# Kernel optimization log

Measured on AMD Instinct MI355X. Metric: run time of the kernel, lower is better.

The kernel has to match this reference:

```python
import jax, jax.numpy as jnp
import numpy as np

NH = 32      # num_attention_heads
HD = 128     # head dim (kv_channels)
NG = 2       # multi_query_group_num
LAYER_NUMBER = 1


def apply_rotary_pos_emb(x, rope_cache):
    # x: [b, np, sq, hn]; rope_cache: [1, sq_max, rot/2, 2]
    b, nh, sq, hn = x.shape
    rot_dim = rope_cache.shape[-2] * 2
    xr, x_pass = x[..., :rot_dim], x[..., rot_dim:]
    xs = xr.reshape(b, nh, sq, rot_dim // 2, 2)
    c = rope_cache[:, :sq].reshape(-1, 1, sq, rot_dim // 2, 2)
    out = jnp.stack(
        [xs[..., 0] * c[..., 0] - xs[..., 1] * c[..., 1],
         xs[..., 1] * c[..., 0] + xs[..., 0] * c[..., 1]], axis=-1)
    out = out.reshape(b, nh, sq, rot_dim)
    return jnp.concatenate([out, x_pass], axis=-1)


def setup_inputs() -> dict:
    key = jax.random.key(0)
    ks = jax.random.split(key, 5)
    b, sq, h = 2, 2048, 4096
    qkv_out = NH * HD + 2 * NG * HD  # 4608
    return {
        "hidden_states": jax.random.normal(ks[0], (b, sq, h), jnp.float32),
        "rope_cache": jax.random.normal(ks[1], (1, sq, HD // 4, 2), jnp.float32),
        "W_qkv": jax.random.normal(ks[2], (h, qkv_out), jnp.float32) * 0.02,
        "b_qkv": jax.random.normal(ks[3], (qkv_out,), jnp.float32) * 0.02,
        "W_dense": jax.random.normal(ks[4], (NH * HD, h), jnp.float32) * 0.02,
    }


def reference(hidden_states, rope_cache, W_qkv, b_qkv, W_dense):
    b, sq, h = hidden_states.shape
    mixed = hidden_states @ W_qkv + b_qkv  # [b, sq, nh*hd + 2*ng*hd]
    q_sz = NH * HD
    kv_sz = NG * HD
    q = mixed[..., :q_sz].reshape(b, sq, NH, HD).transpose(0, 2, 1, 3)          # [b,nh,sq,hd]
    k = mixed[..., q_sz:q_sz + kv_sz].reshape(b, sq, NG, HD).transpose(0, 2, 1, 3)  # [b,ng,sq,hd]
    v = mixed[..., q_sz + kv_sz:].reshape(b, sq, NG, HD).transpose(0, 2, 1, 3)      # [b,ng,sq,hd]

    q = apply_rotary_pos_emb(q, rope_cache)
    k = apply_rotary_pos_emb(k, rope_cache)

    # expand KV groups to full heads (multi-query attention)
    rep = NH // NG
    k = jnp.broadcast_to(k[:, :, None], (b, NG, rep, sq, HD)).reshape(b, NH, sq, HD)
    v = jnp.broadcast_to(v[:, :, None], (b, NG, rep, sq, HD)).reshape(b, NH, sq, HD)

    # CoreAttention (eager path, fp32 softmax, causal)
    coeff = float(max(1, LAYER_NUMBER))  # apply_query_key_layer_scaling
    norm_factor = np.sqrt(HD) * coeff
    scores = jnp.einsum("bhqd,bhkd->bhqk", q, k) / norm_factor
    scores = scores.astype(jnp.float32) * coeff
    causal = jnp.tril(jnp.ones((sq, sq), dtype=bool))
    scores = jnp.where(causal[None, None], scores, -jnp.inf)
    probs = jax.nn.softmax(scores, axis=-1).astype(v.dtype)
    context = jnp.einsum("bhqk,bhkd->bhqd", probs, v)   # [b,nh,sq,hd]
    context = context.transpose(0, 2, 1, 3).reshape(b, sq, NH * HD)
    return context @ W_dense
```

## Files before the change

kernel.cpp:

```cpp
#include <hip/hip_runtime.h>
#include <hip/hip_bf16.h>
#include <stdint.h>

#define B_    2
#define SQ    2048
#define H_    4096
#define NHEAD 32
#define HDIM  128
#define NGRP  2
#define QKVN  4608
#define SCALE 0.08838834764831845f
#define QSCALE (0.08838834764831845f * 1.4426950408889634f)

typedef __attribute__((ext_vector_type(8))) short bf16x8;
typedef __attribute__((ext_vector_type(4))) short bf16x4;
typedef __attribute__((ext_vector_type(4))) float f32x4;

__device__ __forceinline__ float b2f(short s) {
  union { float f; unsigned u; } x; x.u = ((unsigned)(unsigned short)s) << 16; return x.f;
}
__device__ __forceinline__ short f2b(float f) {
  union { float f; unsigned u; } x; x.f = f;
  unsigned r = x.u + 0x7fffu + ((x.u >> 16) & 1u);
  return (short)(r >> 16);
}
__device__ __forceinline__ void gll16(const void* g, void* l) {
  __builtin_amdgcn_global_load_lds(
      (const __attribute__((address_space(1))) unsigned int*)g,
      (__attribute__((address_space(3))) unsigned int*)l, 16, 0, 0);
}

__global__ void conv_f32_bf16(const float* __restrict__ x, short* __restrict__ y, int n) {
  int i = (blockIdx.x * blockDim.x + threadIdx.x) * 4;
  if (i >= n) return;
  float4 v = *(const float4*)(x + i);
  union { short s[4]; uint2 u; } o;
  o.s[0] = f2b(v.x); o.s[1] = f2b(v.y); o.s[2] = f2b(v.z); o.s[3] = f2b(v.w);
  *(uint2*)(y + i) = o.u;
}

__global__ void transpose_f32_bf16(const float* __restrict__ W, short* __restrict__ Wt,
                                   int R, int C) {
  __shared__ float tile[32][33];
  int c0 = blockIdx.x * 32, r0 = blockIdx.y * 32;
  int tx = threadIdx.x, ty = threadIdx.y;
  #pragma unroll
  for (int i = 0; i < 32; i += 8)
    tile[ty + i][tx] = W[(size_t)(r0 + ty + i) * C + c0 + tx];
  __syncthreads();
  #pragma unroll
  for (int i = 0; i < 32; i += 8)
    Wt[(size_t)(c0 + ty + i) * R + r0 + tx] = f2b(tile[tx][ty + i]);
}

template<bool BIAS, bool OUTF32>
__global__ __launch_bounds__(256, 2) void gemm_bf16(
    const short* __restrict__ A, const short* __restrict__ Bt,
    const float* __restrict__ bias, short* __restrict__ outb,
    float* __restrict__ outf, int M, int N, int K)
{
  __shared__ short smA[128 * 64];
  __shared__ short smB[128 * 64];
  const int t = threadIdx.x;
  const int l = t & 63;
  const int w = t >> 6;
  const int wr = w >> 1, wc = w & 1;
  const int m0 = blockIdx.y * 128, n0 = blockIdx.x * 128;

  const f32x4 z = {0.f, 0.f, 0.f, 0.f};
  f32x4 acc[4][4];
  #pragma unroll
  for (int m = 0; m < 4; ++m)
    #pragma unroll
    for (int n = 0; n < 4; ++n) acc[m][n] = z;

  for (int k0 = 0; k0 < K; k0 += 64) {
    __syncthreads();
    #pragma unroll
    for (int i = 0; i < 4; ++i) {
      int c = t + i * 256;
      int row = c >> 3, slot = c & 7;
      int ss = slot ^ (row & 7);
      gll16(A  + (size_t)(m0 + row) * K + k0 + ss * 8,
            (char*)smA + (i * 256 + w * 64) * 16);
      gll16(Bt + (size_t)(n0 + row) * K + k0 + ss * 8,
            (char*)smB + (i * 256 + w * 64) * 16);
    }
    __syncthreads();
    #pragma unroll
    for (int kk = 0; kk < 2; ++kk) {
      bf16x8 a[4], b[4];
      #pragma unroll
      for (int m = 0; m < 4; ++m) {
        int row = wr * 64 + m * 16 + (l & 15);
        int off = (kk * 64 + ((l >> 4) << 4)) ^ ((row & 7) << 4);
        a[m] = *(const bf16x8*)((const char*)smA + row * 128 + off);
      }
      #pragma unroll
      for (int n = 0; n < 4; ++n) {
        int row = wc * 64 + n * 16 + (l & 15);
        int off = (kk * 64 + ((l >> 4) << 4)) ^ ((row & 7) << 4);
        b[n] = *(const bf16x8*)((const char*)smB + row * 128 + off);
      }
      #pragma unroll
      for (int m = 0; m < 4; ++m)
        #pragma unroll
        for (int n = 0; n < 4; ++n)
          acc[m][n] = __builtin_amdgcn_mfma_f32_16x16x32_bf16(a[m], b[n], acc[m][n], 0, 0, 0);
    }
  }

  #pragma unroll
  for (int m = 0; m < 4; ++m) {
    int row = m0 + wr * 64 + m * 16 + ((l >> 4) << 2);
    #pragma unroll
    for (int n = 0; n < 4; ++n) {
      int col = n0 + wc * 64 + n * 16 + (l & 15);
      float bv = BIAS ? bias[col] : 0.f;
      #pragma unroll
      for (int j = 0; j < 4; ++j) {
        float vv = acc[m][n][j] + bv;
        if (OUTF32) outf[(size_t)(row + j) * N + col] = vv;
        else        outb[(size_t)(row + j) * N + col] = f2b(vv);
      }
    }
  }
}

__global__ __launch_bounds__(512, 2) void gemm256(
    const short* __restrict__ A, const short* __restrict__ Bt,
    float* __restrict__ outf, int M, int N, int K, int nbx)
{
  __shared__ char sm[131072];
  const int t = threadIdx.x, l = t & 63, w = t >> 6;
  const int lq = l & 15, hi = l >> 4;
  const int wm = w >> 2, wn = w & 3;
  const int nwg = (int)gridDim.x;
  const int oid = (int)blockIdx.x;
  const int swz = (oid & 7) * (nwg >> 3) + (oid >> 3);
  const int by = swz / nbx, bx = swz - by * nbx;
  const int m0 = by * 256, n0 = bx * 256;
  const int nkt = K >> 6;

  auto stage = [&](int tt, int r) {
    int kb = (tt < nkt ? tt : tt - nkt) << 6;
    const short* src = (r < 2) ? Bt + (size_t)(n0 + (r << 7)) * K + kb
                               : A  + (size_t)(m0 + ((r - 2) << 7)) * K + kb;
    char* dst = sm + ((tt & 1) << 16) + (r >= 2 ? 0 : 32768) + ((r & 1) << 14);
    #pragma unroll
    for (int i = 0; i < 2; ++i) {
      int c = (i << 9) + t;
      int row = c >> 3, ss = (c & 7) ^ (row & 7);
      gll16(src + (size_t)row * K + ss * 8, dst + ((i << 9) + (w << 6)) * 16);
    }
  };
  bf16x8 aC[2][2], bC[4][2];
  auto ldA = [&](int b, int q, bf16x8 (&out)[2][2]) {
    #pragma unroll
    for (int fr = 0; fr < 2; ++fr) {
      int ra = wm * 128 + q * 32 + fr * 16 + lq;
      #pragma unroll
      for (int kk = 0; kk < 2; ++kk)
        out[fr][kk] = *(const bf16x8*)(sm + (b << 16) + ra * 128 + (((kk << 2) + hi) ^ (ra & 7)) * 16);
    }
  };
  auto ldB = [&](int b, bf16x8 (&out)[4][2]) {
    #pragma unroll
    for (int fc = 0; fc < 4; ++fc) {
      int rb = wn * 64 + fc * 16 + lq;
      #pragma unroll
      for (int kk = 0; kk < 2; ++kk)
        out[fc][kk] = *(const bf16x8*)(sm + (b << 16) + 32768 + rb * 128 + (((kk << 2) + hi) ^ (rb & 7)) * 16);
    }
  };

  const f32x4 z = {0.f, 0.f, 0.f, 0.f};
  f32x4 acc[8][4];
  #pragma unroll
  for (int i = 0; i < 8; ++i)
    #pragma unroll
    for (int j = 0; j < 4; ++j) acc[i][j] = z;

  stage(0, 0); stage(0, 1); stage(0, 2); stage(0, 3);
  stage(1, 0); stage(1, 1); stage(1, 2);
  asm volatile("s_waitcnt vmcnt(6)" ::: "memory");
  __builtin_amdgcn_s_barrier();
  ldB(0, bC); ldA(0, 0, aC);
  asm volatile("s_waitcnt lgkmcnt(0)" ::: "memory");

#define GPHASE(p, STG_T, STG_R)                                           \
  {                                                                       \
    stage((STG_T), (STG_R));                                              \
    __builtin_amdgcn_sched_barrier(0);                                    \
    __builtin_amdgcn_s_barrier();                                         \
    __builtin_amdgcn_s_setprio(1);                                        \
    _Pragma("unroll")                                                     \
    for (int kk = 0; kk < 2; ++kk)                                        \
      _Pragma("unroll")                                                   \
      for (int fr = 0; fr < 2; ++fr)                                      \
        _Pragma("unroll")                                                 \
        for (int fc = 0; fc < 4; ++fc)                                    \
          acc[(p) * 2 + fr][fc] = __builtin_amdgcn_mfma_f32_16x16x32_bf16(\
              aC[fr][kk], bC[fc][kk], acc[(p) * 2 + fr][fc], 0, 0, 0);    \
    __builtin_amdgcn_s_setprio(0);                                        \
    if ((p) < 3) ldA(bsel, (p) + 1, aC);                                  \
    else { ldA(bsel ^ 1, 0, aC); ldB(bsel ^ 1, bC); }                     \
    asm volatile("s_waitcnt lgkmcnt(0)" ::: "memory");                    \
    if ((p) == 2) asm volatile("s_waitcnt vmcnt(4)" ::: "memory");        \
    __builtin_amdgcn_s_barrier();                                         \
  }

  for (int tt = 0; tt < nkt; ++tt) {
    const int bsel = tt & 1;
    GPHASE(0, tt + 1, 3)
    GPHASE(1, tt + 2, 0)
    GPHASE(2, tt + 2, 1)
    GPHASE(3, tt + 2, 2)
  }
#undef GPHASE

  #pragma unroll
  for (int q = 0; q < 4; ++q)
    #pragma unroll
    for (int fr = 0; fr < 2; ++fr) {
      int gr0 = m0 + wm * 128 + q * 32 + fr * 16 + hi * 4;
      #pragma unroll
      for (int fc = 0; fc < 4; ++fc) {
        int col = n0 + wn * 64 + fc * 16 + lq;
        #pragma unroll
        for (int j = 0; j < 4; ++j)
          outf[(size_t)(gr0 + j) * N + col] = acc[q * 2 + fr][fc][j];
      }
    }
}

__global__ void rope_split(const short* __restrict__ mixed, const float* __restrict__ rope,
                           short* __restrict__ qo, short* __restrict__ ko, short* __restrict__ vo)
{
  const int CH = QKVN / 8;
  int idx = blockIdx.x * blockDim.x + threadIdx.x;
  if (idx >= B_ * SQ * CH) return;
  int row = idx / CH;
  int cc = (idx - row * CH) * 8;
  int b = row >> 11, s = row & 2047;

  bf16x8 xv = *(const bf16x8*)(mixed + (size_t)row * QKVN + cc);
  float x[8];
  #pragma unroll
  for (int i = 0; i < 8; ++i) x[i] = b2f(xv[i]);

  int sect, hh, d = cc & 127;
  if (cc < 4096)      { sect = 0; hh = cc >> 7; }
  else if (cc < 4352) { sect = 1; hh = (cc - 4096) >> 7; }
  else                { sect = 2; hh = (cc - 4352) >> 7; }

  if (sect < 2 && d < 64) {
    float4 ca = *(const float4*)(rope + s * 64 + d);
    float4 cb = *(const float4*)(rope + s * 64 + d + 4);
    float t0;
    t0 = x[0]*ca.x - x[1]*ca.y; x[1] = x[1]*ca.x + x[0]*ca.y; x[0] = t0;
    t0 = x[2]*ca.z - x[3]*ca.w; x[3] = x[3]*ca.z + x[2]*ca.w; x[2] = t0;
    t0 = x[4]*cb.x - x[5]*cb.y; x[5] = x[5]*cb.x + x[4]*cb.y; x[4] = t0;
    t0 = x[6]*cb.z - x[7]*cb.w; x[7] = x[7]*cb.z + x[6]*cb.w; x[6] = t0;
  }
  if (sect == 0) {
    #pragma unroll
    for (int i = 0; i < 8; ++i) x[i] *= QSCALE;
  }

  short* dst; size_t oidx;
  if (sect == 0)      { dst = qo; oidx = (((size_t)(b * NHEAD + hh) * SQ) + s) * HDIM + d; }
  else if (sect == 1) { dst = ko; oidx = (((size_t)(b * NGRP + hh) * SQ) + s) * HDIM + d; }
  else                { dst = vo; oidx = (((size_t)(b * NGRP + hh) * SQ) + s) * HDIM + d; }
  bf16x8 ov;
  #pragma unroll
  for (int i = 0; i < 8; ++i) ov[i] = f2b(x[i]);
  *(bf16x8*)(dst + oidx) = ov;
}

__global__ __launch_bounds__(512, 2) void attn_fwd(
    const short* __restrict__ q, const short* __restrict__ k,
    const short* __restrict__ v, short* __restrict__ ctx)
{
  __shared__ short smem[8192 + 9216];
  short* smK = smem;
  short* smV = smem + 8192;

  const int h = blockIdx.y, b = blockIdx.z;
  const int g = h >> 4;
  const int t = threadIdx.x, l = t & 63, w = t >> 6;
  const int lq = l & 15, hi = l >> 4;

  const short* qbase = q + ((size_t)(b * NHEAD + h) * SQ) * HDIM;
  const short* kbase = k + ((size_t)(b * NGRP + g) * SQ) * HDIM;
  const short* vbase = v + ((size_t)(b * NGRP + g) * SQ) * HDIM;

  const f32x4 z = {0.f, 0.f, 0.f, 0.f};

  for (int pass = 0; pass < 2; ++pass) {
    const int s = pass ? (7 - (int)blockIdx.x) : (int)blockIdx.x;
    const int q0 = s * 256;
    const int qw = q0 + w * 32;
    const int nkt = 4 * s + 4;

    bf16x8 qf[2][4];
    #pragma unroll
    for (int fq = 0; fq < 2; ++fq)
      #pragma unroll
      for (int kf = 0; kf < 4; ++kf)
        qf[fq][kf] = *(const bf16x8*)(qbase + (size_t)(qw + fq * 16 + lq) * HDIM + kf * 32 + hi * 8);

    f32x4 of[2][8];
    #pragma unroll
    for (int a = 0; a < 2; ++a)
      #pragma unroll
      for (int d = 0; d < 8; ++d) of[a][d] = z;
    float mrow[2] = {-1e30f, -1e30f};
    float lrow[2] = {0.f, 0.f};

    for (int kt = 0; kt < nkt; ++kt) {
      const int kb = kt * 64;
      __syncthreads();
      #pragma unroll
      for (int i = 0; i < 2; ++i) {
        int c = t + i * 512;
        int row = c >> 4, slot = c & 15;
        int ss = slot ^ (row & 7);
        gll16(kbase + (size_t)(kb + row) * HDIM + ss * 8,
              (char*)smK + (i * 512 + w * 64) * 16);
      }
      #pragma unroll
      for (int i = 0; i < 2; ++i) {
        int c = t + i * 512;
        int key = c & 63, d0 = (c >> 6) << 3;
        bf16x8 vv = *(const bf16x8*)(vbase + (size_t)(kb + key) * HDIM + d0);
        #pragma unroll
        for (int jj = 0; jj < 8; ++jj)
          smV[(d0 + jj) * 72 + key] = vv[jj];
      }
      __syncthreads();

      if (kb > qw + 31) continue;

      f32x4 st[2][4];
      #pragma unroll
      for (int fq = 0; fq < 2; ++fq)
        #pragma unroll
        for (int fk = 0; fk < 4; ++fk) st[fq][fk] = z;
      #pragma unroll
      for (int kf = 0; kf < 4; ++kf) {
        bf16x8 kfr[4];
        #pragma unroll
        for (int fk = 0; fk < 4; ++fk) {
          int row = fk * 16 + lq;
          int slot = (kf * 4 + hi) ^ (row & 7);
          kfr[fk] = *(const bf16x8*)((const char*)smK + row * 256 + slot * 16);
        }
        #pragma unroll
        for (int fq = 0; fq < 2; ++fq)
          #pragma unroll
          for (int fk = 0; fk < 4; ++fk)
            st[fq][fk] = __builtin_amdgcn_mfma_f32_16x16x32_bf16(kfr[fk], qf[fq][kf], st[fq][fk], 0, 0, 0);
      }

      bf16x4 pa[2][4];
      #pragma unroll
      for (int fq = 0; fq < 2; ++fq) {
        float sv[16];
        #pragma unroll
        for (int fk = 0; fk < 4; ++fk)
          #pragma unroll
          for (int j = 0; j < 4; ++j) sv[fk * 4 + j] = st[fq][fk][j];
        if (kb + 63 > qw + fq * 16) {
          int qrow = qw + fq * 16 + lq;
          #pragma unroll
          for (int fk = 0; fk < 4; ++fk)
            #pragma unroll
            for (int j = 0; j < 4; ++j)
              if (kb + fk * 16 + hi * 4 + j > qrow) sv[fk * 4 + j] = -1e30f;
        }
        float mx = sv[0];
        #pragma unroll
        for (int i = 1; i < 16; ++i) mx = fmaxf(mx, sv[i]);
        mx = fmaxf(mx, __shfl_xor(mx, 16));
        mx = fmaxf(mx, __shfl_xor(mx, 32));
        if (__any(mx > mrow[fq] + 11.0f)) {
          float mn = fmaxf(mrow[fq], mx);
          float corr = exp2f(mrow[fq] - mn);
          mrow[fq] = mn;
          lrow[fq] *= corr;
          float cj[4];
          #pragma unroll
          for (int j = 0; j < 4; ++j) cj[j] = __shfl(corr, hi * 4 + j);
          #pragma unroll
          for (int df = 0; df < 8; ++df)
            #pragma unroll
            for (int j = 0; j < 4; ++j) of[fq][df][j] *= cj[j];
        }
        float rs = 0.f;
        #pragma unroll
        for (int i = 0; i < 16; ++i) { sv[i] = exp2f(sv[i] - mrow[fq]); rs += sv[i]; }
        rs += __shfl_xor(rs, 16);
        rs += __shfl_xor(rs, 32);
        lrow[fq] += rs;
        #pragma unroll
        for (int fk = 0; fk < 4; ++fk) {
          bf16x4 p;
          p[0] = f2b(sv[fk * 4 + 0]); p[1] = f2b(sv[fk * 4 + 1]);
          p[2] = f2b(sv[fk * 4 + 2]); p[3] = f2b(sv[fk * 4 + 3]);
          pa[fq][fk] = p;
        }
      }

      #pragma unroll
      for (int fk = 0; fk < 4; ++fk) {
        bf16x4 vb[8];
        #pragma unroll
        for (int df = 0; df < 8; ++df)
          vb[df] = *(const bf16x4*)(smV + (df * 16 + lq) * 72 + fk * 16 + hi * 4);
        #pragma unroll
        for (int df = 0; df < 8; ++df) {
          of[0][df] = __builtin_amdgcn_mfma_f32_16x16x16bf16_1k(pa[0][fk], vb[df], of[0][df], 0, 0, 0);
          of[1][df] = __builtin_amdgcn_mfma_f32_16x16x16bf16_1k(pa[1][fk], vb[df], of[1][df], 0, 0, 0);
        }
      }
    }

    #pragma unroll
    for (int fq = 0; fq < 2; ++fq) {
      float inv = 1.f / lrow[fq];
      float ij[4];
      #pragma unroll
      for (int j = 0; j < 4; ++j) ij[j] = __shfl(inv, hi * 4 + j);
      #pragma unroll
      for (int j = 0; j < 4; ++j) {
        int srow = qw + fq * 16 + hi * 4 + j;
        size_t rbase = ((size_t)(b * SQ + srow)) * (NHEAD * HDIM) + (size_t)h * HDIM;
        #pragma unroll
        for (int df = 0; df < 8; ++df)
          ctx[rbase + df * 16 + lq] = f2b(of[fq][df][j] * ij[j]);
      }
    }
    __syncthreads();
  }
}

extern "C" void kernel_launch(void* const* d_in, const int* in_sizes, int n_in,
                              void* d_out, int out_size, void* d_ws, size_t ws_size,
                              hipStream_t stream)
{
  const float* hidden = (const float*)d_in[0];
  const float* rope   = (const float*)d_in[1];
  const float* Wqkv   = (const float*)d_in[2];
  const float* bqkv   = (const float*)d_in[3];
  const float* Wd     = (const float*)d_in[4];
  float* out = (float*)d_out;

  if (ws_size < 113246208ULL) return;
  char* ws = (char*)d_ws;
  short* hsb   = (short*)(ws);
  short* wT    = (short*)(ws + 33554432);
  short* mixed = (short*)(ws + 71303168);
  short* k_r   = (short*)(ws + 109051904);
  short* v_r   = (short*)(ws + 111149056);

  conv_f32_bf16<<<16384, 256, 0, stream>>>(hidden, hsb, B_ * SQ * H_);
  transpose_f32_bf16<<<dim3(QKVN / 32, H_ / 32), dim3(32, 8), 0, stream>>>(Wqkv, wT, H_, QKVN);
  gemm_bf16<true, false><<<dim3(QKVN / 128, (B_ * SQ) / 128), 256, 0, stream>>>(
      hsb, wT, bqkv, mixed, nullptr, B_ * SQ, QKVN, H_);
  rope_split<<<9216, 256, 0, stream>>>(mixed, rope, hsb, k_r, v_r);
  transpose_f32_bf16<<<dim3(H_ / 32, H_ / 32), dim3(32, 8), 0, stream>>>(Wd, wT, H_, H_);
  attn_fwd<<<dim3(4, NHEAD, B_), 512, 0, stream>>>(hsb, k_r, v_r, mixed);
  gemm256<<<256, 512, 0, stream>>>(mixed, wT, out, B_ * SQ, H_, H_, H_ / 256);
}
```

Before: 549.4 us.

## Restructure GEMM pipeline to single-tile prefetch with per-quarter A staging

Changes the 256x256 bf16 GEMM's global-to-LDS staging so each phase loads a quarter of the next k-tile, with the A quarters matched to the rows that phase consumes. The prefetch depth drops from two tiles to one. LDS fragment loads now sit at the start of each phase, before the MFMAs, instead of being issued for the next phase after the MFMAs. This removes the cross-phase lgkm waits and reorders the vmcnt waits, at the risk of exposing LDS latency and reducing global-load lookahead.

```diff
diff --git a/kernel.cpp b/kernel.cpp
--- a/kernel.cpp
+++ b/kernel.cpp
@@ -142,35 +142,38 @@
   const int m0 = by * 256, n0 = bx * 256;
   const int nkt = K >> 6;
 
-  auto stage = [&](int tt, int r) {
+  auto stage = [&](int tt, int u) {
     int kb = (tt < nkt ? tt : tt - nkt) << 6;
-    const short* src = (r < 2) ? Bt + (size_t)(n0 + (r << 7)) * K + kb
-                               : A  + (size_t)(m0 + ((r - 2) << 7)) * K + kb;
-    char* dst = sm + ((tt & 1) << 16) + (r >= 2 ? 0 : 32768) + ((r & 1) << 14);
+    char* buf = sm + ((tt & 1) << 16);
     #pragma unroll
     for (int i = 0; i < 2; ++i) {
       int c = (i << 9) + t;
-      int row = c >> 3, ss = (c & 7) ^ (row & 7);
-      gll16(src + (size_t)row * K + ss * 8, dst + ((i << 9) + (w << 6)) * 16);
+      int grow = (u < 2) ? (c >> 3) + ((u & 1) << 7)
+                         : (c >> 3) + (i << 6) + ((u & 1) << 6);
+      int ss = (c & 7) ^ (grow & 7);
+      const short* src = (u < 2) ? Bt + (size_t)(n0 + grow) * K + kb + ss * 8
+                                 : A  + (size_t)(m0 + grow) * K + kb + ss * 8;
+      gll16(src, buf + (u < 2 ? 32768 : 0) + grow * 128 + (c & 7) * 16);
     }
   };
+
   bf16x8 aC[2][2], bC[4][2];
-  auto ldA = [&](int b, int q, bf16x8 (&out)[2][2]) {
+  auto ldA = [&](int b, int q) {
     #pragma unroll
     for (int fr = 0; fr < 2; ++fr) {
       int ra = wm * 128 + q * 32 + fr * 16 + lq;
       #pragma unroll
       for (int kk = 0; kk < 2; ++kk)
-        out[fr][kk] = *(const bf16x8*)(sm + (b << 16) + ra * 128 + (((kk << 2) + hi) ^ (ra & 7)) * 16);
+        aC[fr][kk] = *(const bf16x8*)(sm + (b << 16) + ra * 128 + (((kk << 2) + hi) ^ (ra & 7)) * 16);
     }
   };
-  auto ldB = [&](int b, bf16x8 (&out)[4][2]) {
+  auto ldB = [&](int b) {
     #pragma unroll
     for (int fc = 0; fc < 4; ++fc) {
       int rb = wn * 64 + fc * 16 + lq;
       #pragma unroll
       for (int kk = 0; kk < 2; ++kk)
-        out[fc][kk] = *(const bf16x8*)(sm + (b << 16) + 32768 + rb * 128 + (((kk << 2) + hi) ^ (rb & 7)) * 16);
+        bC[fc][kk] = *(const bf16x8*)(sm + (b << 16) + 32768 + rb * 128 + (((kk << 2) + hi) ^ (rb & 7)) * 16);
     }
   };
 
@@ -182,16 +185,14 @@
     for (int j = 0; j < 4; ++j) acc[i][j] = z;
 
   stage(0, 0); stage(0, 1); stage(0, 2); stage(0, 3);
-  stage(1, 0); stage(1, 1); stage(1, 2);
-  asm volatile("s_waitcnt vmcnt(6)" ::: "memory");
+  asm volatile("s_waitcnt vmcnt(0)" ::: "memory");
   __builtin_amdgcn_s_barrier();
-  ldB(0, bC); ldA(0, 0, aC);
-  asm volatile("s_waitcnt lgkmcnt(0)" ::: "memory");
-
-#define GPHASE(p, STG_T, STG_R)                                           \
+
+#define GPHASE(Q, VM)                                                     \
   {                                                                       \
-    stage((STG_T), (STG_R));                                              \
-    __builtin_amdgcn_sched_barrier(0);                                    \
+    if ((Q) == 0) ldB(bsel);                                              \
+    ldA(bsel, (Q));                                                       \
+    stage(T + 1, (Q));                                                    \
     __builtin_amdgcn_s_barrier();                                         \
     __builtin_amdgcn_s_setprio(1);                                        \
     _Pragma("unroll")                                                     \
@@ -200,22 +201,20 @@
       for (int fr = 0; fr < 2; ++fr)                                      \
         _Pragma("unroll")                                                 \
         for (int fc = 0; fc < 4; ++fc)                                    \
-          acc[(p) * 2 + fr][fc] = __builtin_amdgcn_mfma_f32_16x16x32_bf16(\
-              aC[fr][kk], bC[fc][kk], acc[(p) * 2 + fr][fc], 0, 0, 0);    \
+          acc[(Q) * 2 + fr][fc] = __builtin_amdgcn_mfma_f32_16x16x32_bf16(\
+              aC[fr][kk], bC[fc][kk], acc[(Q) * 2 + fr][fc], 0, 0, 0);    \
     __builtin_amdgcn_s_setprio(0);                                        \
-    if ((p) < 3) ldA(bsel, (p) + 1, aC);                                  \
-    else { ldA(bsel ^ 1, 0, aC); ldB(bsel ^ 1, bC); }                     \
-    asm volatile("s_waitcnt lgkmcnt(0)" ::: "memory");                    \
-    if ((p) == 2) asm volatile("s_waitcnt vmcnt(4)" ::: "memory");        \
+    if ((VM) == 4) asm volatile("s_waitcnt vmcnt(4)" ::: "memory");       \
+    if ((VM) == 2) asm volatile("s_waitcnt vmcnt(2)" ::: "memory");       \
     __builtin_amdgcn_s_barrier();                                         \
   }
 
-  for (int tt = 0; tt < nkt; ++tt) {
-    const int bsel = tt & 1;
-    GPHASE(0, tt + 1, 3)
-    GPHASE(1, tt + 2, 0)
-    GPHASE(2, tt + 2, 1)
-    GPHASE(3, tt + 2, 2)
+  for (int T = 0; T < nkt; ++T) {
+    const int bsel = T & 1;
+    GPHASE(0, -1)
+    GPHASE(1, 4)
+    GPHASE(2, -1)
+    GPHASE(3, 2)
   }
 #undef GPHASE
 
```

Result: faster. 535.5 us (-2.5%).
